# Kernel optimization log

Measured on AMD Instinct MI355X. Metric: run time of the kernel, lower is better.

The kernel has to match this reference:

```python
import jax, jax.numpy as jnp
import numpy as np

B, S, H, D = 1, 2048, 16, 64
IN = 1024
STATE = H * D          # 1024
OUT = 1024
N_LAYERS = 24
EPS = 1e-6


def _rms(t):
    # RMSNorm without affine over last dim
    return t * jax.lax.rsqrt(jnp.mean(t * t, axis=-1, keepdims=True) + EPS)


def setup_inputs() -> dict:
    key = jax.random.key(0)
    ks = jax.random.split(key, 6)
    std = 0.02
    return {
        "x": jax.random.normal(ks[0], (B, S, IN), jnp.float32),
        # input_projection.weight^T: [in, 5*state]  (q|k|v|f|gate)
        "W_in": jax.random.normal(ks[1], (IN, 5 * STATE), jnp.float32) * std,
        "state_weight": jax.random.normal(ks[2], (H, D, D), jnp.float32) * std,
        "forget_multiplier": jax.random.normal(ks[3], (H, D), jnp.float32) * std,
        "logistic_factor": jnp.zeros((H,), jnp.float32),
        "g_norm_weight": jnp.ones((STATE,), jnp.float32),
        "W_out": jax.random.normal(ks[4], (STATE, OUT), jnp.float32) * (std / np.sqrt(2 * N_LAYERS)),
    }


def reference(x, W_in, state_weight, forget_multiplier, logistic_factor, g_norm_weight, W_out):
    proj = x @ W_in                                        # [B,S,5*STATE]
    q, k, v, f, gate = jnp.split(proj, [STATE, 2 * STATE, 3 * STATE, 4 * STATE], axis=-1)
    q = _rms(q.reshape(B, S, H, D))
    k = _rms(k.reshape(B, S, H, D))
    v = _rms(v.reshape(B, S, H, D))
    f = f.reshape(B, S, H, D)

    factor = jax.nn.sigmoid(logistic_factor)               # [H]
    # kvT[b,s,h,i,j] = k_i * (v_j * factor_h)
    kv = k[..., :, None] * (v * factor[None, None, :, None])[..., None, :]   # [B,S,H,D,D]
    # forget gate input, row-wise (depends on k-index i only)
    fg = jax.nn.sigmoid(f * (2.0 * jax.nn.sigmoid(forget_multiplier)))       # [B,S,H,D]
    rg = jax.nn.sigmoid(jnp.asarray(20.0, x.dtype))        # reset_input hardcoded to 20 -> ~1
    W = state_weight * factor[:, None, None]               # [H,D,D]

    def step(state, inp):
        kv_t, f_t = inp                                    # [B,H,D,D], [B,H,D]
        state = f_t[..., None] * jnp.einsum('bhik,hkj->bhij', state, W) + rg * kv_t
        return state, state

    xs = (kv.transpose(1, 0, 2, 3, 4), fg.transpose(1, 0, 2, 3))
    state0 = jnp.zeros((B, H, D, D), x.dtype)
    _, states = jax.lax.scan(step, state0, xs)             # [S,B,H,D,D]

    o = jnp.einsum('bshi,sbhij->bshj', q, states).reshape(B, S, STATE)
    y = o * jax.nn.silu(gate)
    y = _rms(y) * g_norm_weight                            # g_norm (affine RMSNorm)
    return y @ W_out
```

## Files before the change

kernel.cpp:

```cpp
#include <hip/hip_runtime.h>
#include <hip/hip_bf16.h>
#include <cstdint>


typedef __attribute__((ext_vector_type(8))) short short8;
typedef __attribute__((ext_vector_type(4))) short short4v;
typedef __attribute__((ext_vector_type(4))) float f32x4;

#define S_  2048
#define H_  16
#define NPROJ_ 5120

__device__ __forceinline__ float bf2f(unsigned short u) {
  unsigned int x = ((unsigned int)u) << 16;
  return __builtin_bit_cast(float, x);
}
__device__ __forceinline__ unsigned short f2bf(float f) {
  unsigned int x = __builtin_bit_cast(unsigned int, f);
  unsigned int r = (x + 0x7fffu + ((x >> 16) & 1u)) >> 16;
  return (unsigned short)r;
}
__device__ __forceinline__ float sigm(float x) { return 1.f / (1.f + __expf(-x)); }

__device__ __forceinline__ void gload_lds16(unsigned short* lds, const unsigned short* g) {
  __builtin_amdgcn_global_load_lds(
      (const __attribute__((address_space(1))) unsigned int*)g,
      (__attribute__((address_space(3))) unsigned int*)lds, 16, 0, 0);
}

__global__ __launch_bounds__(256) void k_prep(const float* __restrict__ x,
                                              const float* __restrict__ Win,
                                              const float* __restrict__ Wout,
                                              const float* __restrict__ sw,
                                              const float* __restrict__ lf,
                                              unsigned short* __restrict__ xbf,
                                              unsigned short* __restrict__ WinT,
                                              unsigned short* __restrict__ WoutT,
                                              unsigned short* __restrict__ Wt,
                                              float* __restrict__ rowsum) {
  const int b = blockIdx.x, tid = threadIdx.x;
  if (b < 1536) {
    __shared__ float tile[64][65];
    const float* src; unsigned short* dst; int C, idx;
    if (b < 1280) { src = Win; dst = WinT; C = 5120; idx = b; }
    else          { src = Wout; dst = WoutT; C = 1024; idx = b - 1280; }
    const int R = 1024;
    int nct = C >> 6;
    int bc = idx % nct, br = idx / nct;
    int r0 = br * 64, c0 = bc * 64;
    int col = tid & 63, q = tid >> 6;
#pragma unroll
    for (int i = 0; i < 16; ++i) {
      int row = q * 16 + i;
      tile[row][col] = src[(size_t)(r0 + row) * C + c0 + col];
    }
    __syncthreads();
#pragma unroll
    for (int i = 0; i < 16; ++i) {
      int crow = q * 16 + i;
      dst[(size_t)(c0 + crow) * R + r0 + col] = f2bf(tile[col][crow]);
    }
  } else if (b < 2560) {
    int i = ((b - 1536) * 256 + tid) * 8;
    float4 v0 = *reinterpret_cast<const float4*>(x + i);
    float4 v1 = *reinterpret_cast<const float4*>(x + i + 4);
    uint4 o;
    o.x = (unsigned)f2bf(v0.x) | ((unsigned)f2bf(v0.y) << 16);
    o.y = (unsigned)f2bf(v0.z) | ((unsigned)f2bf(v0.w) << 16);
    o.z = (unsigned)f2bf(v1.x) | ((unsigned)f2bf(v1.y) << 16);
    o.w = (unsigned)f2bf(v1.z) | ((unsigned)f2bf(v1.w) << 16);
    *reinterpret_cast<uint4*>(xbf + i) = o;
  } else if (b < 2576) {
    int h = b - 2560;
    float factor = sigm(lf[h]);
    int j = tid >> 2, kq = (tid & 3) << 4;
#pragma unroll 4
    for (int k = kq; k < kq + 16; ++k)
      Wt[((size_t)h * 64 + j) * 64 + k] = f2bf(sw[((size_t)h * 64 + k) * 64 + j] * factor);
  } else {
#pragma unroll
    for (int i = 0; i < 8; ++i) rowsum[tid * 8 + i] = 0.f;
  }
}

__global__ __launch_bounds__(256) void k_gemm1_fused(
    const unsigned short* __restrict__ A, const unsigned short* __restrict__ BT,
    const float* __restrict__ fm, const float* __restrict__ lf,
    unsigned short* __restrict__ qnb, unsigned short* __restrict__ knb,
    unsigned short* __restrict__ vtb, unsigned short* __restrict__ fgb,
    unsigned short* __restrict__ sgb) {
  __shared__ __attribute__((aligned(16))) unsigned short As[3][128 * 32];
  __shared__ __attribute__((aligned(16))) unsigned short Bs[3][128 * 32];
  const int K = 1024;
  const int tid = threadIdx.x, w = tid >> 6, l = tid & 63;
  const int bx = blockIdx.x;
  const int m0 = (bx / 40) * 128, n0 = (bx % 40) * 128;
  const int wrow = (w >> 1) * 64, wcol = (w & 1) * 64;
  const int l15 = l & 15, lq = l >> 4;
  const int swzoff = l15 * 32 + ((lq ^ ((l15 >> 1) & 3)) * 8);
  f32x4 acc[4][4] = {};
  const int c0 = w * 2;
  const int srow0 = c0 * 16 + (l >> 2);
  const int scol = ((l & 3) ^ ((l >> 3) & 3)) * 8;
  const unsigned short* ga0 = A + (size_t)(m0 + srow0) * K + scol;
  const unsigned short* ga1 = ga0 + 16 * K;
  const unsigned short* gb0 = BT + (size_t)(n0 + srow0) * K + scol;
  const unsigned short* gb1 = gb0 + 16 * K;
#define STAGE1(bufi, kof)                                  \
  do {                                                     \
    gload_lds16(&As[bufi][c0 * 512], ga0 + (kof));         \
    gload_lds16(&As[bufi][(c0 + 1) * 512], ga1 + (kof));   \
    gload_lds16(&Bs[bufi][c0 * 512], gb0 + (kof));         \
    gload_lds16(&Bs[bufi][(c0 + 1) * 512], gb1 + (kof));   \
  } while (0)
  STAGE1(0, 0);
  STAGE1(1, 32);
  asm volatile("s_waitcnt vmcnt(4)" ::: "memory");
  __builtin_amdgcn_s_barrier();
  asm volatile("" ::: "memory");
  for (int t = 0; t < 32; ++t) {
    const unsigned short* Ab = As[t % 3];
    const unsigned short* Bb = Bs[t % 3];
    short8 af[4], bfr[4];
#pragma unroll
    for (int mt = 0; mt < 4; ++mt)
      af[mt] = *reinterpret_cast<const short8*>(Ab + (4 * (w >> 1) + mt) * 512 + swzoff);
#pragma unroll
    for (int nt = 0; nt < 4; ++nt)
      bfr[nt] = *reinterpret_cast<const short8*>(Bb + (4 * (w & 1) + nt) * 512 + swzoff);
    __builtin_amdgcn_s_setprio(1);
#pragma unroll
    for (int mt = 0; mt < 4; ++mt)
#pragma unroll
      for (int nt = 0; nt < 2; ++nt)
        acc[mt][nt] = __builtin_amdgcn_mfma_f32_16x16x32_bf16(af[mt], bfr[nt], acc[mt][nt], 0, 0, 0);
    __builtin_amdgcn_s_setprio(0);
    __builtin_amdgcn_sched_barrier(0);
    if (t < 30) STAGE1((t + 2) % 3, (t + 2) * 32);
    __builtin_amdgcn_sched_barrier(0);
    __builtin_amdgcn_s_setprio(1);
#pragma unroll
    for (int mt = 0; mt < 4; ++mt)
#pragma unroll
      for (int nt = 2; nt < 4; ++nt)
        acc[mt][nt] = __builtin_amdgcn_mfma_f32_16x16x32_bf16(af[mt], bfr[nt], acc[mt][nt], 0, 0, 0);
    __builtin_amdgcn_s_setprio(0);
    if (t < 30) {
      asm volatile("s_waitcnt vmcnt(4)" ::: "memory");
      __builtin_amdgcn_s_barrier();
      asm volatile("" ::: "memory");
    } else if (t == 30) {
      asm volatile("s_waitcnt vmcnt(0)" ::: "memory");
      __builtin_amdgcn_s_barrier();
      asm volatile("" ::: "memory");
    }
  }
  const int seg = n0 >> 10;
  const int colbase = n0 + wcol;
  const int h = (colbase & 1023) >> 6;
  const float rg = 0.9999999979388464f;
  if (seg < 3) {
    float sc = 1.f;
    if (seg == 2) sc = rg * sigm(lf[h]);
    unsigned short* dst = (seg == 0 ? qnb : (seg == 1 ? knb : vtb)) + (size_t)h * S_ * 64;
#pragma unroll
    for (int mt = 0; mt < 4; ++mt) {
      float rstd[4];
#pragma unroll
      for (int r = 0; r < 4; ++r) {
        float s = 0.f;
#pragma unroll
        for (int nt = 0; nt < 4; ++nt) s += acc[mt][nt][r] * acc[mt][nt][r];
        s += __shfl_xor(s, 1); s += __shfl_xor(s, 2);
        s += __shfl_xor(s, 4); s += __shfl_xor(s, 8);
        rstd[r] = rsqrtf(s * (1.f / 64.f) + 1e-6f) * sc;
      }
#pragma unroll
      for (int nt = 0; nt < 4; ++nt)
#pragma unroll
        for (int r = 0; r < 4; ++r) {
          int sr = m0 + wrow + 16 * mt + lq * 4 + r;
          dst[(size_t)sr * 64 + 16 * nt + l15] = f2bf(acc[mt][nt][r] * rstd[r]);
        }
    }
  } else if (seg == 3) {
    float mult[4];
#pragma unroll
    for (int nt = 0; nt < 4; ++nt) mult[nt] = 2.f * sigm(fm[h * 64 + 16 * nt + l15]);
    unsigned short* dst = fgb + (size_t)h * S_ * 64;
#pragma unroll
    for (int mt = 0; mt < 4; ++mt)
#pragma unroll
      for (int nt = 0; nt < 4; ++nt)
#pragma unroll
        for (int r = 0; r < 4; ++r) {
          int sr = m0 + wrow + 16 * mt + lq * 4 + r;
          dst[(size_t)sr * 64 + 16 * nt + l15] = f2bf(sigm(acc[mt][nt][r] * mult[nt]));
        }
  } else {
    int j0 = colbase - 4096;
#pragma unroll
    for (int mt = 0; mt < 4; ++mt)
#pragma unroll
      for (int nt = 0; nt < 4; ++nt)
#pragma unroll
        for (int r = 0; r < 4; ++r) {
          int sr = m0 + wrow + 16 * mt + lq * 4 + r;
          float g = acc[mt][nt][r];
          sgb[(size_t)sr * 1024 + j0 + 16 * nt + l15] = f2bf(g * sigm(g));
        }
  }
}

#define TS 64
#define HALO 5
#define WIN 69
#define VWROWS 80
#define KSTR 72
#define PMAX 5

__global__ __launch_bounds__(256) void k_recur(const unsigned short* __restrict__ qnb,
                                               const unsigned short* __restrict__ knb,
                                               const unsigned short* __restrict__ vtb,
                                               const unsigned short* __restrict__ fgb,
                                               const unsigned short* __restrict__ Wt,
                                               const unsigned short* __restrict__ sgb,
                                               const float* __restrict__ gnw,
                                               float* __restrict__ rowsum,
                                               unsigned short* __restrict__ ubuf) {
  __shared__ __attribute__((aligned(16))) unsigned short kw[WIN * KSTR];
  __shared__ __attribute__((aligned(16))) unsigned short fw[WIN * KSTR];
  __shared__ __attribute__((aligned(16))) unsigned short vw[2][VWROWS * KSTR];
  const int bx = blockIdx.x;
  const int h = bx & 15, tile = bx >> 4;
  const int s0 = tile * TS;
  const int tid = threadIdx.x, w = tid >> 6, l = tid & 63;

  short8 aw[2];
#pragma unroll
  for (int kt = 0; kt < 2; ++kt)
    aw[kt] = *reinterpret_cast<const short8*>(
        Wt + ((size_t)h * 64 + 16 * w + (l & 15)) * 64 + 32 * kt + 8 * (l >> 4));

  const unsigned short* kh = knb + (size_t)h * S_ * 64;
  const unsigned short* fh = fgb + (size_t)h * S_ * 64;
  const unsigned short* vh = vtb + (size_t)h * S_ * 64;
  const short8 z8 = {0, 0, 0, 0, 0, 0, 0, 0};
  for (int e = tid; e < WIN * 8; e += 256) {
    int rw = e >> 3, c8 = (e & 7) << 3;
    int t = s0 - HALO + rw;
    short8 kv8 = z8, fv8 = z8, vv8 = z8;
    if (t >= 0) {
      kv8 = *reinterpret_cast<const short8*>(kh + (size_t)t * 64 + c8);
      fv8 = *reinterpret_cast<const short8*>(fh + (size_t)t * 64 + c8);
      vv8 = *reinterpret_cast<const short8*>(vh + (size_t)t * 64 + c8);
    }
    *reinterpret_cast<short8*>(kw + rw * KSTR + c8) = kv8;
    *reinterpret_cast<short8*>(fw + rw * KSTR + c8) = fv8;
    *reinterpret_cast<short8*>(vw[0] + rw * KSTR + c8) = vv8;
  }
  for (int e = tid; e < (VWROWS - WIN) * 8; e += 256) {
    int rw = WIN + (e >> 3), c8 = (e & 7) << 3;
    *reinterpret_cast<short8*>(vw[0] + rw * KSTR + c8) = z8;
  }

  const int srow = tid >> 2, t4 = tid & 3;
  float qc[16], oacc[16];
  {
    const unsigned short* qrow = qnb + ((size_t)h * S_ + s0 + srow) * 64 + t4 * 16;
    short8 qa = *reinterpret_cast<const short8*>(qrow);
    short8 qb = *reinterpret_cast<const short8*>(qrow + 8);
#pragma unroll
    for (int i = 0; i < 8; ++i) { qc[i] = bf2f((unsigned short)qa[i]); oacc[i] = 0.f; }
#pragma unroll
    for (int i = 0; i < 8; ++i) { qc[8 + i] = bf2f((unsigned short)qb[i]); oacc[8 + i] = 0.f; }
  }
  __syncthreads();

  for (int p = 0; p <= PMAX; ++p) {
    const unsigned short* cur = vw[p & 1];
    if (p > 0) {
      const unsigned short* fr = fw + (srow - p + HALO + 1) * KSTR + t4 * 16;
      short8 a = *reinterpret_cast<const short8*>(fr);
      short8 b = *reinterpret_cast<const short8*>(fr + 8);
#pragma unroll
      for (int i = 0; i < 8; ++i) qc[i] *= bf2f((unsigned short)a[i]);
#pragma unroll
      for (int i = 0; i < 8; ++i) qc[8 + i] *= bf2f((unsigned short)b[i]);
    }
    {
      int rr = srow - p + HALO;
      const unsigned short* kr = kw + rr * KSTR + t4 * 16;
      short8 a = *reinterpret_cast<const short8*>(kr);
      short8 b = *reinterpret_cast<const short8*>(kr + 8);
      float part = 0.f;
#pragma unroll
      for (int i = 0; i < 8; ++i) part += qc[i] * bf2f((unsigned short)a[i]);
#pragma unroll
      for (int i = 0; i < 8; ++i) part += qc[8 + i] * bf2f((unsigned short)b[i]);
      part += __shfl_xor(part, 1);
      part += __shfl_xor(part, 2);
      const unsigned short* vr = cur + rr * KSTR + t4 * 16;
      short8 va = *reinterpret_cast<const short8*>(vr);
      short8 vb = *reinterpret_cast<const short8*>(vr + 8);
#pragma unroll
      for (int i = 0; i < 8; ++i) oacc[i] += part * bf2f((unsigned short)va[i]);
#pragma unroll
      for (int i = 0; i < 8; ++i) oacc[8 + i] += part * bf2f((unsigned short)vb[i]);
    }
    if (p < PMAX) {
      unsigned short* nxt = vw[(p + 1) & 1];
#pragma unroll
      for (int nt = 0; nt < 5; ++nt) {
        f32x4 a = {0.f, 0.f, 0.f, 0.f};
#pragma unroll
        for (int kt = 0; kt < 2; ++kt) {
          short8 bfrag = *reinterpret_cast<const short8*>(
              cur + (16 * nt + (l & 15)) * KSTR + 32 * kt + 8 * (l >> 4));
          a = __builtin_amdgcn_mfma_f32_16x16x32_bf16(aw[kt], bfrag, a, 0, 0, 0);
        }
        int trow = 16 * nt + (l & 15);
        short4v pk;
        pk[0] = (short)f2bf(a[0]); pk[1] = (short)f2bf(a[1]);
        pk[2] = (short)f2bf(a[2]); pk[3] = (short)f2bf(a[3]);
        *reinterpret_cast<short4v*>(nxt + trow * KSTR + 16 * w + 4 * (l >> 4)) = pk;
      }
    }
    __syncthreads();
  }
  const int scol0 = h * 64 + t4 * 16;
  const int srowg = s0 + srow;
  const unsigned short* sgrow = sgb + (size_t)srowg * 1024 + scol0;
  short8 g1 = *reinterpret_cast<const short8*>(sgrow);
  short8 g2 = *reinterpret_cast<const short8*>(sgrow + 8);
  float u[16];
  float part = 0.f;
#pragma unroll
  for (int i = 0; i < 8; ++i) { u[i] = oacc[i] * bf2f((unsigned short)g1[i]); part += u[i] * u[i]; }
#pragma unroll
  for (int i = 0; i < 8; ++i) { u[8 + i] = oacc[8 + i] * bf2f((unsigned short)g2[i]); part += u[8 + i] * u[8 + i]; }
  part += __shfl_xor(part, 1);
  part += __shfl_xor(part, 2);
  if (t4 == 0) atomicAdd(rowsum + srowg, part);
  const float* gp = gnw + scol0;
  short8 o1, o2;
#pragma unroll
  for (int i = 0; i < 8; ++i) { o1[i] = (short)f2bf(u[i] * gp[i]); o2[i] = (short)f2bf(u[8 + i] * gp[8 + i]); }
  unsigned short* od = ubuf + (size_t)srowg * 1024 + scol0;
  *reinterpret_cast<short8*>(od) = o1;
  *reinterpret_cast<short8*>(od + 8) = o2;
}

__global__ __launch_bounds__(256) void k_gemm2(const unsigned short* __restrict__ A,
                                               const unsigned short* __restrict__ BT,
                                               const float* __restrict__ rowsum,
                                               float* __restrict__ C) {
  __shared__ __attribute__((aligned(16))) unsigned short As[3][64 * 64];
  __shared__ __attribute__((aligned(16))) unsigned short Bs[3][64 * 64];
  const int K = 1024;
  const int tid = threadIdx.x, w = tid >> 6, l = tid & 63;
  const int bx = blockIdx.x;
  const int m0 = (bx >> 4) * 64, n0 = (bx & 15) * 64;
  const int wrow = (w >> 1) * 32, wcol = (w & 1) * 32;
  const int l15 = l & 15, lq = l >> 4;
  const int swzoff = l15 * 32 + ((lq ^ ((l15 >> 1) & 3)) * 8);
  f32x4 acc[2][2] = {};
  const int scol = ((l & 3) ^ ((l >> 3) & 3)) * 8;
  const unsigned short* gsp[4]; int dofs[4]; int isB[4];
#pragma unroll
  for (int j = 0; j < 4; ++j) {
    int id = 4 * w + j;
    int mid = id & 7;
    int kk = mid >> 2, g = mid & 3;
    isB[j] = id >> 3;
    dofs[j] = mid * 512;
    const unsigned short* base = (id < 8) ? A : BT;
    int r0 = (id < 8) ? m0 : n0;
    gsp[j] = base + (size_t)(r0 + 16 * g + (l >> 2)) * K + kk * 32 + scol;
  }
#define STAGE2(bufi, kof)                                                          \
  do {                                                                             \
    gload_lds16((isB[0] ? &Bs[bufi][0] : &As[bufi][0]) + dofs[0], gsp[0] + (kof)); \
    gload_lds16((isB[1] ? &Bs[bufi][0] : &As[bufi][0]) + dofs[1], gsp[1] + (kof)); \
    gload_lds16((isB[2] ? &Bs[bufi][0] : &As[bufi][0]) + dofs[2], gsp[2] + (kof)); \
    gload_lds16((isB[3] ? &Bs[bufi][0] : &As[bufi][0]) + dofs[3], gsp[3] + (kof)); \
  } while (0)
  STAGE2(0, 0);
  STAGE2(1, 64);
  asm volatile("s_waitcnt vmcnt(4)" ::: "memory");
  __builtin_amdgcn_s_barrier();
  asm volatile("" ::: "memory");
  for (int t = 0; t < 16; ++t) {
    if (t < 14) STAGE2((t + 2) % 3, (t + 2) * 64);
    const unsigned short* Ab = As[t % 3];
    const unsigned short* Bb = Bs[t % 3];
#pragma unroll
    for (int kk = 0; kk < 2; ++kk) {
      short8 af[2], bfr[2];
#pragma unroll
      for (int mt = 0; mt < 2; ++mt)
        af[mt] = *reinterpret_cast<const short8*>(
            Ab + (kk * 4 + 2 * (w >> 1) + mt) * 512 + swzoff);
#pragma unroll
      for (int nt = 0; nt < 2; ++nt)
        bfr[nt] = *reinterpret_cast<const short8*>(
            Bb + (kk * 4 + 2 * (w & 1) + nt) * 512 + swzoff);
#pragma unroll
      for (int mt = 0; mt < 2; ++mt)
#pragma unroll
        for (int nt = 0; nt < 2; ++nt)
          acc[mt][nt] = __builtin_amdgcn_mfma_f32_16x16x32_bf16(af[mt], bfr[nt], acc[mt][nt], 0, 0, 0);
    }
    if (t < 14) {
      asm volatile("s_waitcnt vmcnt(4)" ::: "memory");
      __builtin_amdgcn_s_barrier();
      asm volatile("" ::: "memory");
    } else if (t == 14) {
      asm volatile("s_waitcnt vmcnt(0)" ::: "memory");
      __builtin_amdgcn_s_barrier();
      asm volatile("" ::: "memory");
    }
  }
#pragma unroll
  for (int mt = 0; mt < 2; ++mt)
#pragma unroll
    for (int r = 0; r < 4; ++r) {
      int row = m0 + wrow + 16 * mt + lq * 4 + r;
      float scl = rsqrtf(rowsum[row] * (1.f / 1024.f) + 1e-6f);
#pragma unroll
      for (int nt = 0; nt < 2; ++nt)
        C[(size_t)row * 1024 + n0 + wcol + 16 * nt + l15] = acc[mt][nt][r] * scl;
    }
}

extern "C" void kernel_launch(void* const* d_in, const int* in_sizes, int n_in,
                              void* d_out, int out_size, void* d_ws, size_t ws_size,
                              hipStream_t stream) {
  const float* x    = (const float*)d_in[0];
  const float* Win  = (const float*)d_in[1];
  const float* sw   = (const float*)d_in[2];
  const float* fm   = (const float*)d_in[3];
  const float* lf   = (const float*)d_in[4];
  const float* gnw  = (const float*)d_in[5];
  const float* Wout = (const float*)d_in[6];
  float* out = (float*)d_out;

  uint8_t* ws = (uint8_t*)d_ws;
  size_t off = 0;
  auto alloc = [&](size_t bytes) -> void* {
    void* p = ws + off;
    off += (bytes + 255) & ~(size_t)255;
    return p;
  };
  unsigned short* xbf   = (unsigned short*)alloc((size_t)S_ * 1024 * 2);
  unsigned short* WinT  = (unsigned short*)alloc((size_t)NPROJ_ * 1024 * 2);
  unsigned short* WoutT = (unsigned short*)alloc((size_t)1024 * 1024 * 2);
  unsigned short* Wt    = (unsigned short*)alloc((size_t)16 * 64 * 64 * 2);
  unsigned short* qnb = (unsigned short*)alloc((size_t)H_ * S_ * 64 * 2);
  unsigned short* knb = (unsigned short*)alloc((size_t)H_ * S_ * 64 * 2);
  unsigned short* vtb = (unsigned short*)alloc((size_t)H_ * S_ * 64 * 2);
  unsigned short* fgb = (unsigned short*)alloc((size_t)H_ * S_ * 64 * 2);
  unsigned short* sgb = (unsigned short*)alloc((size_t)S_ * 1024 * 2);
  unsigned short* ubuf = (unsigned short*)alloc((size_t)S_ * 1024 * 2);
  float* rowsum = (float*)alloc((size_t)S_ * 4);

  k_prep<<<dim3(2577), dim3(256), 0, stream>>>(x, Win, Wout, sw, lf, xbf, WinT, WoutT, Wt,
                                               rowsum);
  k_gemm1_fused<<<dim3(16 * 40), dim3(256), 0, stream>>>(xbf, WinT, fm, lf,
                                                         qnb, knb, vtb, fgb, sgb);
  k_recur<<<dim3((S_ / TS) * H_), dim3(256), 0, stream>>>(qnb, knb, vtb, fgb, Wt,
                                                          sgb, gnw, rowsum, ubuf);
  k_gemm2<<<dim3(32 * 16), dim3(256), 0, stream>>>(ubuf, WoutT, rowsum, out);
}
```

Baseline: 69.69 us.

## Switch gemm1 to double-buffered BK=64 pipeline with fewer barriers

```diff
diff --git a/kernel.cpp b/kernel.cpp
--- a/kernel.cpp
+++ b/kernel.cpp
@@ -89,8 +89,8 @@
     unsigned short* __restrict__ qnb, unsigned short* __restrict__ knb,
     unsigned short* __restrict__ vtb, unsigned short* __restrict__ fgb,
     unsigned short* __restrict__ sgb) {
-  __shared__ __attribute__((aligned(16))) unsigned short As[3][128 * 32];
-  __shared__ __attribute__((aligned(16))) unsigned short Bs[3][128 * 32];
+  __shared__ __attribute__((aligned(16))) unsigned short As[2][128 * 64];
+  __shared__ __attribute__((aligned(16))) unsigned short Bs[2][128 * 64];
   const int K = 1024;
   const int tid = threadIdx.x, w = tid >> 6, l = tid & 63;
   const int bx = blockIdx.x;
@@ -99,57 +99,54 @@
   const int l15 = l & 15, lq = l >> 4;
   const int swzoff = l15 * 32 + ((lq ^ ((l15 >> 1) & 3)) * 8);
   f32x4 acc[4][4] = {};
-  const int c0 = w * 2;
-  const int srow0 = c0 * 16 + (l >> 2);
   const int scol = ((l & 3) ^ ((l >> 3) & 3)) * 8;
-  const unsigned short* ga0 = A + (size_t)(m0 + srow0) * K + scol;
-  const unsigned short* ga1 = ga0 + 16 * K;
-  const unsigned short* gb0 = BT + (size_t)(n0 + srow0) * K + scol;
-  const unsigned short* gb1 = gb0 + 16 * K;
-#define STAGE1(bufi, kof)                                  \
-  do {                                                     \
-    gload_lds16(&As[bufi][c0 * 512], ga0 + (kof));         \
-    gload_lds16(&As[bufi][(c0 + 1) * 512], ga1 + (kof));   \
-    gload_lds16(&Bs[bufi][c0 * 512], gb0 + (kof));         \
-    gload_lds16(&Bs[bufi][(c0 + 1) * 512], gb1 + (kof));   \
+  const unsigned short* gsp[8]; int dofs[8]; int isB[8];
+#pragma unroll
+  for (int j = 0; j < 8; ++j) {
+    int id = 8 * w + j;
+    int mid = id & 15;
+    int kk = mid >> 3, g = mid & 7;
+    isB[j] = id >> 4;
+    dofs[j] = mid * 512;
+    const unsigned short* base = isB[j] ? BT : A;
+    int r0 = isB[j] ? n0 : m0;
+    gsp[j] = base + (size_t)(r0 + 16 * g + (l >> 2)) * K + kk * 32 + scol;
+  }
+#define STAGE1(bufi, kof)                                                            \
+  do {                                                                               \
+    _Pragma("unroll")                                                                \
+    for (int j = 0; j < 8; ++j)                                                      \
+      gload_lds16((isB[j] ? &Bs[bufi][0] : &As[bufi][0]) + dofs[j], gsp[j] + (kof)); \
   } while (0)
   STAGE1(0, 0);
-  STAGE1(1, 32);
-  asm volatile("s_waitcnt vmcnt(4)" ::: "memory");
+  asm volatile("s_waitcnt vmcnt(0)" ::: "memory");
   __builtin_amdgcn_s_barrier();
   asm volatile("" ::: "memory");
-  for (int t = 0; t < 32; ++t) {
-    const unsigned short* Ab = As[t % 3];
-    const unsigned short* Bb = Bs[t % 3];
-    short8 af[4], bfr[4];
-#pragma unroll
-    for (int mt = 0; mt < 4; ++mt)
-      af[mt] = *reinterpret_cast<const short8*>(Ab + (4 * (w >> 1) + mt) * 512 + swzoff);
-#pragma unroll
-    for (int nt = 0; nt < 4; ++nt)
-      bfr[nt] = *reinterpret_cast<const short8*>(Bb + (4 * (w & 1) + nt) * 512 + swzoff);
-    __builtin_amdgcn_s_setprio(1);
-#pragma unroll
-    for (int mt = 0; mt < 4; ++mt)
-#pragma unroll
-      for (int nt = 0; nt < 2; ++nt)
-        acc[mt][nt] = __builtin_amdgcn_mfma_f32_16x16x32_bf16(af[mt], bfr[nt], acc[mt][nt], 0, 0, 0);
-    __builtin_amdgcn_s_setprio(0);
+  for (int t = 0; t < 16; ++t) {
+    if (t < 15) STAGE1((t + 1) & 1, (t + 1) * 64);
     __builtin_amdgcn_sched_barrier(0);
-    if (t < 30) STAGE1((t + 2) % 3, (t + 2) * 32);
-    __builtin_amdgcn_sched_barrier(0);
-    __builtin_amdgcn_s_setprio(1);
-#pragma unroll
-    for (int mt = 0; mt < 4; ++mt)
-#pragma unroll
-      for (int nt = 2; nt < 4; ++nt)
-        acc[mt][nt] = __builtin_amdgcn_mfma_f32_16x16x32_bf16(af[mt], bfr[nt], acc[mt][nt], 0, 0, 0);
-    __builtin_amdgcn_s_setprio(0);
-    if (t < 30) {
-      asm volatile("s_waitcnt vmcnt(4)" ::: "memory");
-      __builtin_amdgcn_s_barrier();
-      asm volatile("" ::: "memory");
-    } else if (t == 30) {
+    const unsigned short* Ab = As[t & 1];
+    const unsigned short* Bb = Bs[t & 1];
+#pragma unroll
+    for (int kk = 0; kk < 2; ++kk) {
+      short8 af[4], bfr[4];
+#pragma unroll
+      for (int mt = 0; mt < 4; ++mt)
+        af[mt] = *reinterpret_cast<const short8*>(
+            Ab + (kk * 8 + 4 * (w >> 1) + mt) * 512 + swzoff);
+#pragma unroll
+      for (int nt = 0; nt < 4; ++nt)
+        bfr[nt] = *reinterpret_cast<const short8*>(
+            Bb + (kk * 8 + 4 * (w & 1) + nt) * 512 + swzoff);
+      __builtin_amdgcn_s_setprio(1);
+#pragma unroll
+      for (int mt = 0; mt < 4; ++mt)
+#pragma unroll
+        for (int nt = 0; nt < 4; ++nt)
+          acc[mt][nt] = __builtin_amdgcn_mfma_f32_16x16x32_bf16(af[mt], bfr[nt], acc[mt][nt], 0, 0, 0);
+      __builtin_amdgcn_s_setprio(0);
+    }
+    if (t < 15) {
       asm volatile("s_waitcnt vmcnt(0)" ::: "memory");
       __builtin_amdgcn_s_barrier();
       asm volatile("" ::: "memory");
```

After: 71.43 us. +2.5%, slower.
